# Kernel tuning notes

Hardware: AMD Instinct MI355X
Metric: run time of the kernel (lower is better)

The kernel has to match this reference:

```python
import jax, jax.numpy as jnp
import numpy as np

L, H, DK, DV, D, DH, V, S, B = 2, 12, 64, 64, 768, 3072, 32000, 1024, 2


def _layernorm(x):
    # matches custom LayerNorm: mean over last dim, biased std, no eps, no affine
    mu = jnp.mean(x, axis=-1, keepdims=True)
    sigma = jnp.sqrt(jnp.mean(jnp.square(x - mu), axis=-1, keepdims=True))
    return (x - mu) / sigma


def setup_inputs() -> dict:
    key = jax.random.key(0)
    ks = jax.random.split(key, 12)
    n = lambda k, shp: (0.02 * jax.random.normal(k, shp, dtype=jnp.float32))
    return {
        "x": jax.random.randint(ks[0], (B, S), 0, V),
        "ignore": jax.random.randint(ks[1], (B, S), 0, 2).astype(jnp.int32),
        "emb": n(ks[2], (V, D)),
        "pos": n(ks[3], (S, D)),
        "Wq": n(ks[4], (L, H, D, DK)), "bq": jnp.zeros((L, H, DK), jnp.float32),
        "Wk": n(ks[5], (L, H, D, DK)), "bk": jnp.zeros((L, H, DK), jnp.float32),
        "Wv": n(ks[6], (L, H, D, DV)), "bv": jnp.zeros((L, H, DV), jnp.float32),
        "Wo": n(ks[7], (L, H * DV, D)), "bo": jnp.zeros((L, D), jnp.float32),
        "W1": n(ks[8], (L, D, DH)), "b1": jnp.zeros((L, DH), jnp.float32),
        "W2": n(ks[9], (L, DH, D)), "b2": jnp.zeros((L, D), jnp.float32),
        "Wout": n(ks[10], (D, V)), "bout": jnp.zeros((V,), jnp.float32),
    }


def reference(x, ignore, emb, pos, Wq, bq, Wk, bk, Wv, bv, Wo, bo, W1, b1, W2, b2, Wout, bout):
    b, s = x.shape
    ign0 = (ignore == 0)  # True = valid token
    # token emb + position emb zeroed on ignored positions (dropout = eval/identity)
    h = emb[x] + pos[None, :, :] * ign0[:, :, None].astype(emb.dtype)

    # mask[b,i,j]: attend iff j<=i AND (ignore[j]==0 OR i==j)  (diagonal always kept)
    causal = jnp.tril(jnp.ones((s, s), dtype=bool))
    eye = jnp.eye(s, dtype=bool)
    allow = (ign0[:, None, None, :] | eye[None, None, :, :]) & causal[None, None, :, :]  # [b,1,i,j]

    scale = jnp.sqrt(jnp.asarray(DK, h.dtype))
    for l in range(L):
        q = jnp.einsum('bsd,hdk->bhsk', h, Wq[l]) + bq[l][None, :, None, :]
        k = jnp.einsum('bsd,hdk->bhsk', h, Wk[l]) + bk[l][None, :, None, :]
        v = jnp.einsum('bsd,hdv->bhsv', h, Wv[l]) + bv[l][None, :, None, :]
        scores = jnp.einsum('bhik,bhjk->bhij', q, k) / scale
        scores = jnp.where(allow, scores, -jnp.inf)
        p = jax.nn.softmax(scores, axis=-1)
        sa = jnp.einsum('bhij,bhjv->bhiv', p, v)
        sa = sa.transpose(0, 2, 1, 3).reshape(b, s, H * DV)  # concat heads (head-major order matches torch cat)
        attn_out = sa @ Wo[l] + bo[l]
        z = _layernorm(h + attn_out)
        # NOTE: original FeedForwardLayer applies GELU AFTER linear2 (faithful to source)
        f = jax.nn.gelu((z @ W1[l] + b1[l]) @ W2[l] + b2[l], approximate=False)
        h = _layernorm(z + f)
    return h @ Wout + bout
```

## Files before the change

kernel.cpp:

```cpp
#include <hip/hip_runtime.h>
#include <math.h>

static constexpr int L_ = 2, H_ = 12, D_ = 768, DH_ = 3072, V_ = 32000,
                     S_ = 1024, B_ = 2;
static constexpr int M_ = B_ * S_;

typedef __attribute__((ext_vector_type(4))) float f32x4;
typedef __attribute__((ext_vector_type(8))) short s16x8;
typedef __attribute__((ext_vector_type(2))) unsigned int u32x2;
typedef __attribute__((ext_vector_type(4))) unsigned int u32x4;

__device__ __forceinline__ unsigned short f2bf(float f) {
    unsigned u = __builtin_bit_cast(unsigned, f);
    u = (u + 0x7FFFu + ((u >> 16) & 1u)) >> 16;
    return (unsigned short)u;
}
__device__ __forceinline__ unsigned pack2(float a, float b) {
    return (unsigned)f2bf(a) | ((unsigned)f2bf(b) << 16);
}

__device__ __forceinline__ void gld16(const void* g, void* l) {
    __builtin_amdgcn_global_load_lds(
        (const __attribute__((address_space(1))) unsigned int*)g,
        (__attribute__((address_space(3))) unsigned int*)l, 16, 0, 0);
}

__global__ __launch_bounds__(256) void wtr_kernel(
    const float* __restrict__ in, unsigned short* __restrict__ out, int K, int N)
{
    __shared__ unsigned short t[64 * 68];
    const size_t mo = (size_t)blockIdx.z * K * N;
    in  += mo; out += mo;
    const int n0 = blockIdx.x * 64, k0 = blockIdx.y * 64;
    const int tid = threadIdx.x;
    const int kr = tid >> 2, nc = (tid & 3) * 16;
    const float* src = in + (size_t)(k0 + kr) * N + n0 + nc;
    #pragma unroll
    for (int j = 0; j < 4; ++j) {
        const float4 v = *(const float4*)(src + j * 4);
        *(u32x2*)&t[kr * 68 + nc + j * 4] = (u32x2){pack2(v.x, v.y), pack2(v.z, v.w)};
    }
    __syncthreads();
    const int nr = tid >> 2, kc = (tid & 3) * 16;
    unsigned short v16[16];
    #pragma unroll
    for (int j = 0; j < 16; ++j) v16[j] = t[(kc + j) * 68 + nr];
    unsigned short* dst = out + (size_t)(n0 + nr) * K + k0 + kc;
    ((u32x4*)dst)[0] = *(u32x4*)&v16[0];
    ((u32x4*)dst)[1] = *(u32x4*)&v16[8];
}

__global__ __launch_bounds__(256) void wtr3_kernel(
    const float* __restrict__ Wq, const float* __restrict__ Wk,
    const float* __restrict__ Wv, unsigned short* __restrict__ oq,
    unsigned short* __restrict__ ok, unsigned short* __restrict__ ov)
{
    __shared__ unsigned short t[64 * 68];
    const int z = blockIdx.z;
    const int which = z / 24, zz = z - which * 24;
    const float* in = (which == 0) ? Wq : (which == 1) ? Wk : Wv;
    unsigned short* out = (which == 0) ? oq : (which == 1) ? ok : ov;
    const size_t mo = (size_t)zz * D_ * 64;
    in += mo; out += mo;
    const int k0 = blockIdx.y * 64;
    const int tid = threadIdx.x;
    const int kr = tid >> 2, nc = (tid & 3) * 16;
    const float* src = in + (size_t)(k0 + kr) * 64 + nc;
    #pragma unroll
    for (int j = 0; j < 4; ++j) {
        const float4 v = *(const float4*)(src + j * 4);
        *(u32x2*)&t[kr * 68 + nc + j * 4] = (u32x2){pack2(v.x, v.y), pack2(v.z, v.w)};
    }
    __syncthreads();
    const int nr = tid >> 2, kc = (tid & 3) * 16;
    unsigned short v16[16];
    #pragma unroll
    for (int j = 0; j < 16; ++j) v16[j] = t[(kc + j) * 68 + nr];
    unsigned short* dst = out + (size_t)nr * D_ + k0 + kc;
    ((u32x4*)dst)[0] = *(u32x4*)&v16[0];
    ((u32x4*)dst)[1] = *(u32x4*)&v16[8];
}

__device__ __forceinline__ void xcd_decode(int& bx, int& by) {
    const int gx = gridDim.x, gy = gridDim.y;
    const int nwg = gx * gy;
    const int flat = blockIdx.y * gx + blockIdx.x;
    const int s = (flat & 7) * (nwg >> 3) + (flat >> 3);
    bx = s / gy;
    by = s % gy;
}

__device__ __forceinline__ void bt64_body(
    const unsigned short* __restrict__ A, const unsigned short* __restrict__ BT,
    const float* __restrict__ bias, void* __restrict__ Cp,
    int N, int K, int act, int k0off, int klen, int bx, int by)
{
    __shared__ unsigned short AB[12288];
    unsigned short* As = AB;
    unsigned short* Bs = AB + 4096;
    const int tid = threadIdx.x;
    const int l = tid & 63, w = tid >> 6;
    const int lq = l & 15, lg = l >> 4;
    const int brow = by * 64, bn = bx * 128;

    f32x4 acc[4][2];
    #pragma unroll
    for (int i = 0; i < 4; ++i)
        #pragma unroll
        for (int j = 0; j < 2; ++j) acc[i][j] = (f32x4)0.f;

    const int arow = tid >> 3;
    const int aq   = (tid & 7) ^ (arow & 7);
    const unsigned short* Abase = A  + (size_t)(brow + arow) * K + k0off + aq * 8;
    const unsigned short* Bbase = BT + (size_t)(bn   + arow) * K + k0off + aq * 8;

    for (int k0 = 0; k0 < klen; k0 += 64) {
        #pragma unroll
        for (int r = 0; r < 2; ++r)
            gld16(Abase + (size_t)r * 32 * K + k0, (char*)As + r * 4096 + tid * 16);
        #pragma unroll
        for (int r = 0; r < 4; ++r)
            gld16(Bbase + (size_t)r * 32 * K + k0, (char*)Bs + r * 4096 + tid * 16);
        __syncthreads();

        #pragma unroll
        for (int kk = 0; kk < 2; ++kk) {
            s16x8 af[4], bf[2];
            #pragma unroll
            for (int mf = 0; mf < 4; ++mf) {
                const int row = mf * 16 + lq;
                const int gg  = (kk * 4 + lg) ^ (row & 7);
                af[mf] = *(const s16x8*)((const char*)As + row * 128 + gg * 16);
            }
            #pragma unroll
            for (int nf = 0; nf < 2; ++nf) {
                const int col = w * 32 + nf * 16 + lq;
                const int gg  = (kk * 4 + lg) ^ (col & 7);
                bf[nf] = *(const s16x8*)((const char*)Bs + col * 128 + gg * 16);
            }
            #pragma unroll
            for (int mf = 0; mf < 4; ++mf)
                #pragma unroll
                for (int nf = 0; nf < 2; ++nf)
                    acc[mf][nf] = __builtin_amdgcn_mfma_f32_16x16x32_bf16(
                        af[mf], bf[nf], acc[mf][nf], 0, 0, 0);
        }
        __syncthreads();
    }

    if (act == 3) {
        #pragma unroll
        for (int nf = 0; nf < 2; ++nf) {
            const int c = w * 32 + nf * 16 + lq;
            const float bb = bias[bn + c];
            #pragma unroll
            for (int mf = 0; mf < 4; ++mf) {
                const int srel = mf * 16 + lg * 4;
                u32x2 pk;
                pk[0] = pack2(acc[mf][nf][0] + bb, acc[mf][nf][1] + bb);
                pk[1] = pack2(acc[mf][nf][2] + bb, acc[mf][nf][3] + bb);
                const int byo = (c * 128 + srel * 2) ^ ((c & 7) << 4);
                *(u32x2*)((char*)AB + byo) = pk;
            }
        }
        __syncthreads();
        const int row = tid >> 1, half = tid & 1;
        const int gcf = bn + row;
        const int head = gcf >> 6, d = gcf & 63;
        const int b = brow >> 10;
        const int sb = (brow & (S_ - 1)) + half * 32;
        unsigned short* dst = (unsigned short*)Cp +
            (((size_t)b * H_ + head) * 64 + d) * S_ + sb;
        #pragma unroll
        for (int u = 0; u < 4; ++u) {
            const int byo = (row * 128 + half * 64 + u * 16) ^ ((row & 7) << 4);
            ((u32x4*)dst)[u] = *(const u32x4*)((const char*)AB + byo);
        }
        return;
    }
    #pragma unroll
    for (int nf = 0; nf < 2; ++nf) {
        const int gcol = bn + w * 32 + nf * 16 + lq;
        const float bb = (act == 4) ? 0.f : bias[gcol];
        #pragma unroll
        for (int mf = 0; mf < 4; ++mf)
            #pragma unroll
            for (int rg = 0; rg < 4; ++rg) {
                const int grow = brow + mf * 16 + lg * 4 + rg;
                float vv = acc[mf][nf][rg] + bb;
                if (act == 1) vv = 0.5f * vv * (1.0f + erff(vv * 0.70710678118654752f));
                if (act == 2)
                    ((unsigned short*)Cp)[(size_t)grow * N + gcol] = f2bf(vv);
                else
                    ((float*)Cp)[(size_t)grow * N + gcol] = vv;
            }
    }
}

__global__ __launch_bounds__(256) void gemm_bt64(
    const unsigned short* __restrict__ A, const unsigned short* __restrict__ BT,
    const float* __restrict__ bias, void* __restrict__ C, int N, int K, int act)
{
    int bx, by; xcd_decode(bx, by);
    bt64_body(A, BT, bias, C, N, K, act, 0, K, bx, by);
}

__global__ __launch_bounds__(256) void gemm_qkv64(
    const unsigned short* __restrict__ A,
    const unsigned short* __restrict__ qT, const unsigned short* __restrict__ kT,
    const unsigned short* __restrict__ vT,
    const float* __restrict__ bq, const float* __restrict__ bk, const float* __restrict__ bv,
    unsigned short* __restrict__ q, unsigned short* __restrict__ k,
    unsigned short* __restrict__ v)
{
    const unsigned short* BT; const float* bi; unsigned short* C; int act;
    if (blockIdx.z == 0)      { BT = qT; bi = bq; C = q; act = 2; }
    else if (blockIdx.z == 1) { BT = kT; bi = bk; C = k; act = 2; }
    else                      { BT = vT; bi = bv; C = v; act = 3; }
    int bx, by; xcd_decode(bx, by);
    bt64_body(A, BT, bi, C, 768, 768, act, 0, 768, bx, by);
}

__global__ __launch_bounds__(256) void gemm_w2sk(
    const unsigned short* __restrict__ A, const unsigned short* __restrict__ BT,
    const float* __restrict__ bias, float* __restrict__ C0, float* __restrict__ C1)
{
    int bx, by; xcd_decode(bx, by);
    if (blockIdx.z == 0)
        bt64_body(A, BT, bias, C0, 768, DH_, 0, 0, 1536, bx, by);
    else
        bt64_body(A, BT, bias, C1, 768, DH_, 4, 1536, 1536, bx, by);
}

__global__ __launch_bounds__(256) void gemm_wosk(
    const unsigned short* __restrict__ A, const unsigned short* __restrict__ BT,
    const float* __restrict__ bias, float* __restrict__ C0, float* __restrict__ C1)
{
    int bx, by; xcd_decode(bx, by);
    if (blockIdx.z == 0)
        bt64_body(A, BT, bias, C0, 768, 768, 0, 0, 384, bx, by);
    else
        bt64_body(A, BT, bias, C1, 768, 768, 4, 384, 384, bx, by);
}

__global__ __launch_bounds__(512, 2) void gemm_deep(
    const unsigned short* __restrict__ A, const unsigned short* __restrict__ BT,
    const float* __restrict__ bias, float* __restrict__ C, int N, int K)
{
    __shared__ char lds[131072];
    const int tid = threadIdx.x;
    const int l = tid & 63, w = tid >> 6;
    const int wr = w >> 2, wc = w & 3;
    const int lq = l & 15, lg = l >> 4;

    int bx, by;
    {
        const int gx = gridDim.x, gy = gridDim.y;
        const int nwg = gx * gy;
        const int flat = blockIdx.y * gx + blockIdx.x;
        const int s = (flat & 7) * (nwg >> 3) + (flat >> 3);
        bx = s / gy; by = s % gy;
    }
    const int brow = by * 256, bn = bx * 256;
    const int NT = K >> 6;

    const int srow = (w << 3) + (l >> 3);
    const int sgr  = (l & 7) ^ (l >> 3);
    const size_t soff = (size_t)srow * K + sgr * 8;
    const unsigned short* Ag = A  + (size_t)brow * K + soff;
    const unsigned short* Bg = BT + (size_t)bn   * K + soff;
    const size_t r64  = (size_t)64 * K;
    const size_t r128 = (size_t)128 * K;
    char* const dA = lds + w * 1024;
    char* const dB = lds + 65536 + w * 1024;

#define STG_A(CB, HF, KT) do {                                                   \
    gld16(Ag + (size_t)(HF) * r128 + (size_t)(KT) * 64,                          \
          dA + (CB) * 32768 + (HF) * 16384);                                     \
    gld16(Ag + (size_t)(HF) * r128 + r64 + (size_t)(KT) * 64,                    \
          dA + (CB) * 32768 + (HF) * 16384 + 8192); } while (0)
#define STG_B(CB, HF, KT) do {                                                   \
    gld16(Bg + (size_t)(HF) * r128 + (size_t)(KT) * 64,                          \
          dB + (CB) * 32768 + (HF) * 16384);                                     \
    gld16(Bg + (size_t)(HF) * r128 + r64 + (size_t)(KT) * 64,                    \
          dB + (CB) * 32768 + (HF) * 16384 + 8192); } while (0)

    f32x4 acc[8][4];
    #pragma unroll
    for (int i = 0; i < 8; ++i)
        #pragma unroll
        for (int j = 0; j < 4; ++j) acc[i][j] = (f32x4)0.f;

    STG_A(0, 0, 0); STG_A(0, 1, 0); STG_B(0, 0, 0); STG_B(0, 1, 0);
    STG_A(1, 0, 1); STG_B(1, 0, 1);
    asm volatile("s_waitcnt vmcnt(4)" ::: "memory");
    __builtin_amdgcn_s_barrier();

    for (int t = 0; t < NT; ++t) {
        const int c = t & 1;
        const char* Ab = lds + c * 32768;
        const char* Bb = lds + 65536 + c * 32768;
        s16x8 af[4], bf[4];

        #pragma unroll
        for (int mf = 0; mf < 4; ++mf) {
            const int row = wr * 128 + mf * 16 + lq;
            af[mf] = *(const s16x8*)(Ab + row * 128 + ((lg ^ (row & 7)) << 4));
        }
        #pragma unroll
        for (int nf = 0; nf < 4; ++nf) {
            const int col = wc * 64 + nf * 16 + lq;
            bf[nf] = *(const s16x8*)(Bb + col * 128 + ((lg ^ (col & 7)) << 4));
        }
        if (t + 1 < NT) STG_A(c ^ 1, 1, t + 1);
        asm volatile("s_waitcnt lgkmcnt(0)" ::: "memory");
        __builtin_amdgcn_sched_barrier(0);
        __builtin_amdgcn_s_barrier();
        __builtin_amdgcn_s_setprio(1);
        #pragma unroll
        for (int mf = 0; mf < 4; ++mf)
            #pragma unroll
            for (int nf = 0; nf < 4; ++nf)
                acc[mf][nf] = __builtin_amdgcn_mfma_f32_16x16x32_bf16(
                    af[mf], bf[nf], acc[mf][nf], 0, 0, 0);
        __builtin_amdgcn_s_setprio(0);
        __builtin_amdgcn_s_barrier();

        #pragma unroll
        for (int mf = 0; mf < 4; ++mf) {
            const int row = wr * 128 + (mf + 4) * 16 + lq;
            af[mf] = *(const s16x8*)(Ab + row * 128 + ((lg ^ (row & 7)) << 4));
        }
        if (t + 1 < NT) STG_B(c ^ 1, 1, t + 1);
        asm volatile("s_waitcnt lgkmcnt(0)" ::: "memory");
        __builtin_amdgcn_sched_barrier(0);
        __builtin_amdgcn_s_barrier();
        __builtin_amdgcn_s_setprio(1);
        #pragma unroll
        for (int mf = 0; mf < 4; ++mf)
            #pragma unroll
            for (int nf = 0; nf < 4; ++nf)
                acc[mf + 4][nf] = __builtin_amdgcn_mfma_f32_16x16x32_bf16(
                    af[mf], bf[nf], acc[mf + 4][nf], 0, 0, 0);
        __builtin_amdgcn_s_setprio(0);
        __builtin_amdgcn_s_barrier();

        #pragma unroll
        for (int mf = 0; mf < 4; ++mf) {
            const int row = wr * 128 + mf * 16 + lq;
            af[mf] = *(const s16x8*)(Ab + row * 128 + (((4 + lg) ^ (row & 7)) << 4));
        }
        #pragma unroll
        for (int nf = 0; nf < 4; ++nf) {
            const int col = wc * 64 + nf * 16 + lq;
            bf[nf] = *(const s16x8*)(Bb + col * 128 + (((4 + lg) ^ (col & 7)) << 4));
        }
        asm volatile("s_waitcnt lgkmcnt(0)" ::: "memory");
        __builtin_amdgcn_sched_barrier(0);
        __builtin_amdgcn_s_barrier();
        __builtin_amdgcn_s_setprio(1);
        #pragma unroll
        for (int mf = 0; mf < 4; ++mf)
            #pragma unroll
            for (int nf = 0; nf < 4; ++nf)
                acc[mf][nf] = __builtin_amdgcn_mfma_f32_16x16x32_bf16(
                    af[mf], bf[nf], acc[mf][nf], 0, 0, 0);
        __builtin_amdgcn_s_setprio(0);
        __builtin_amdgcn_s_barrier();

        #pragma unroll
        for (int mf = 0; mf < 4; ++mf) {
            const int row = wr * 128 + (mf + 4) * 16 + lq;
            af[mf] = *(const s16x8*)(Ab + row * 128 + (((4 + lg) ^ (row & 7)) << 4));
        }
        asm volatile("s_waitcnt lgkmcnt(0)" ::: "memory");
        __builtin_amdgcn_sched_barrier(0);
        __builtin_amdgcn_s_barrier();
        __builtin_amdgcn_s_setprio(1);
        #pragma unroll
        for (int mf = 0; mf < 4; ++mf)
            #pragma unroll
            for (int nf = 0; nf < 4; ++nf)
                acc[mf + 4][nf] = __builtin_amdgcn_mfma_f32_16x16x32_bf16(
                    af[mf], bf[nf], acc[mf + 4][nf], 0, 0, 0);
        __builtin_amdgcn_s_setprio(0);

        if (t + 2 < NT) {
            STG_A(c, 0, t + 2); STG_B(c, 0, t + 2);
            asm volatile("s_waitcnt vmcnt(4)" ::: "memory");
            __builtin_amdgcn_s_barrier();
        } else if (t + 1 < NT) {
            asm volatile("s_waitcnt vmcnt(0)" ::: "memory");
            __builtin_amdgcn_s_barrier();
        }
    }
#undef STG_A
#undef STG_B

    #pragma unroll
    for (int nf = 0; nf < 4; ++nf) {
        const int gcol = bn + wc * 64 + nf * 16 + lq;
        const float bb = bias[gcol];
        #pragma unroll
        for (int mf = 0; mf < 8; ++mf)
            #pragma unroll
            for (int rg = 0; rg < 4; ++rg) {
                const int grow = brow + wr * 128 + mf * 16 + lg * 4 + rg;
                C[(size_t)grow * N + gcol] = acc[mf][nf][rg] + bb;
            }
    }
}

__global__ __launch_bounds__(256) void gemm_f32b(
    const unsigned short* __restrict__ A, const float* __restrict__ B,
    const float* __restrict__ bias, float* __restrict__ C, int N, int K)
{
    __shared__ unsigned short As[8192];
    __shared__ unsigned short Bs[8192];
    const int tid = threadIdx.x;
    const int l   = tid & 63, wid = tid >> 6;
    const int wr  = wid >> 1, wc = wid & 1;
    const int brow = blockIdx.y * 128, bn = blockIdx.x * 128;
    f32x4 acc[4][4];
    #pragma unroll
    for (int i = 0; i < 4; ++i)
        #pragma unroll
        for (int j = 0; j < 4; ++j) acc[i][j] = (f32x4)0.f;
    const int arow = tid >> 3;
    const int aq   = (tid & 7) ^ (arow & 7);
    const int bkq  = tid >> 5, bnq = tid & 31;
    for (int k0 = 0; k0 < K; k0 += 64) {
        #pragma unroll
        for (int r = 0; r < 4; ++r)
            gld16(A + (size_t)(brow + r * 32 + arow) * K + k0 + aq * 8,
                  (char*)As + r * 4096 + wid * 1024);
        #pragma unroll
        for (int r = 0; r < 2; ++r) {
            const int kb = r * 32 + bkq * 4;
            const float* pp = B + (size_t)(k0 + kb) * N + bn + bnq * 4;
            const float4 v0 = *(const float4*)(pp);
            const float4 v1 = *(const float4*)(pp + N);
            const float4 v2 = *(const float4*)(pp + 2 * (size_t)N);
            const float4 v3 = *(const float4*)(pp + 3 * (size_t)N);
            const int g = kb >> 3, bytek = (kb & 4) * 2;
            const float* f0 = (const float*)&v0; const float* f1 = (const float*)&v1;
            const float* f2 = (const float*)&v2; const float* f3 = (const float*)&v3;
            #pragma unroll
            for (int i = 0; i < 4; ++i) {
                const int n = bnq * 4 + i;
                char* dst = (char*)Bs + n * 128 + ((g ^ (n & 7)) * 16) + bytek;
                *(u32x2*)dst = (u32x2){pack2(f0[i], f1[i]), pack2(f2[i], f3[i])};
            }
        }
        __syncthreads();
        #pragma unroll
        for (int kk = 0; kk < 2; ++kk) {
            s16x8 af[4], bf[4];
            #pragma unroll
            for (int mf = 0; mf < 4; ++mf) {
                const int row = wr * 64 + mf * 16 + (l & 15);
                const int gg  = (kk * 4 + (l >> 4)) ^ (row & 7);
                af[mf] = *(const s16x8*)((const char*)As + row * 128 + gg * 16);
            }
            #pragma unroll
            for (int nf = 0; nf < 4; ++nf) {
                const int col = wc * 64 + nf * 16 + (l & 15);
                const int gg  = (kk * 4 + (l >> 4)) ^ (col & 7);
                bf[nf] = *(const s16x8*)((const char*)Bs + col * 128 + gg * 16);
            }
            #pragma unroll
            for (int mf = 0; mf < 4; ++mf)
                #pragma unroll
                for (int nf = 0; nf < 4; ++nf)
                    acc[mf][nf] = __builtin_amdgcn_mfma_f32_16x16x32_bf16(
                        af[mf], bf[nf], acc[mf][nf], 0, 0, 0);
        }
        __syncthreads();
    }
    const int lr = l >> 4, lc = l & 15;
    #pragma unroll
    for (int nf = 0; nf < 4; ++nf) {
        const int gcol = bn + wc * 64 + nf * 16 + lc;
        const float bb = bias[gcol];
        #pragma unroll
        for (int mf = 0; mf < 4; ++mf)
            #pragma unroll
            for (int rg = 0; rg < 4; ++rg) {
                const int grow = brow + wr * 64 + mf * 16 + lr * 4 + rg;
                C[(size_t)grow * N + gcol] = acc[mf][nf][rg] + bb;
            }
    }
}

__global__ __launch_bounds__(256) void fattn_kernel(
    const unsigned short* __restrict__ qm, const unsigned short* __restrict__ km,
    const unsigned short* __restrict__ vt, const int* __restrict__ ign,
    unsigned short* __restrict__ sab)
{
    __shared__ unsigned short Ks[2][4096];
    __shared__ unsigned short VTs[2][4096];
    __shared__ float addvs[2][64];
    __shared__ unsigned short PTs[4][1024];

    const int hh = blockIdx.y, b = blockIdx.z;
    const int zy = b * 12 + hh;
    const int qt = (zy >= 16) ? (15 - blockIdx.x) : blockIdx.x;

    const int tid = threadIdx.x;
    const int l = tid & 63, w = tid >> 6;
    const int g = l >> 4, lq = l & 15;
    const int i = qt * 64 + w * 16 + lq;

    const size_t qgb = ((size_t)(b * S_ + i)) * D_ + hh * 64;
    const s16x8 qf0 = *(const s16x8*)(qm + qgb + g * 8);
    const s16x8 qf1 = *(const s16x8*)(qm + qgb + 32 + g * 8);

    f32x4 accO[4];
    #pragma unroll
    for (int d = 0; d < 4; ++d) accO[d] = (f32x4)0.f;
    float mrun = -1e30f, lrun = 0.f;

    const int srow = tid >> 3, sg = tid & 7;
    const size_t kbase = (size_t)(b * S_) * D_ + hh * 64;
    const size_t vbase = ((size_t)(b * H_ + hh) * 64) * S_;

    auto stage = [&](int t, int bufi) {
        const int j0 = t * 64;
        #pragma unroll
        for (int r = 0; r < 2; ++r) {
            const int row = r * 32 + srow;
            const int gsw = (sg ^ (row & 7)) * 8;
            gld16(km + kbase + (size_t)(j0 + row) * D_ + gsw,
                  (char*)&Ks[bufi][0] + (r * 256 + tid) * 16);
            gld16(vt + vbase + (size_t)row * S_ + j0 + gsw,
                  (char*)&VTs[bufi][0] + (r * 256 + tid) * 16);
        }
        if (tid < 64)
            addvs[bufi][tid] = (ign[b * S_ + j0 + tid] == 0) ? 0.f : -INFINITY;
    };

    stage(0, 0);
    asm volatile("s_waitcnt vmcnt(0) lgkmcnt(0)" ::: "memory");
    __syncthreads();

    for (int t = 0; t <= qt; ++t) {
        const int cur = t & 1;
        const int j0 = t * 64;
        if (t < qt) stage(t + 1, cur ^ 1);

        f32x4 adv[4];
        #pragma unroll
        for (int kf = 0; kf < 4; ++kf)
            adv[kf] = *(const f32x4*)&addvs[cur][kf * 16 + g * 4];

        f32x4 sacc[4];
        #pragma unroll
        for (int kf = 0; kf < 4; ++kf) sacc[kf] = (f32x4)0.f;
        __builtin_amdgcn_s_setprio(1);
        #pragma unroll
        for (int kk = 0; kk < 2; ++kk) {
            const s16x8 qv = kk ? qf1 : qf0;
            #pragma unroll
            for (int kf = 0; kf < 4; ++kf) {
                const int row = kf * 16 + lq;
                const s16x8 kv = *(const s16x8*)((const char*)&Ks[cur][0] + row * 128 +
                                                 (((kk * 4 + g) ^ (row & 7)) * 16));
                sacc[kf] = __builtin_amdgcn_mfma_f32_16x16x32_bf16(kv, qv, sacc[kf], 0, 0, 0);
            }
        }
        __builtin_amdgcn_s_setprio(0);

        float tmax = -INFINITY;
        if (t < qt) {
            #pragma unroll
            for (int kf = 0; kf < 4; ++kf)
                #pragma unroll
                for (int rg = 0; rg < 4; ++rg) {
                    const float s = fmaf(sacc[kf][rg], 0.125f, adv[kf][rg]);
                    sacc[kf][rg] = s;
                    tmax = fmaxf(tmax, s);
                }
        } else {
            #pragma unroll
            for (int kf = 0; kf < 4; ++kf)
                #pragma unroll
                for (int rg = 0; rg < 4; ++rg) {
                    const int j = j0 + kf * 16 + g * 4 + rg;
                    const float sv = sacc[kf][rg] * 0.125f;
                    const float s = (j > i) ? -INFINITY
                                  : (j == i ? sv : sv + adv[kf][rg]);
                    sacc[kf][rg] = s;
                    tmax = fmaxf(tmax, s);
                }
        }
        tmax = fmaxf(tmax, __shfl_xor(tmax, 16));
        tmax = fmaxf(tmax, __shfl_xor(tmax, 32));
        const float mnew = fmaxf(mrun, tmax);
        const float fac = __expf(mrun - mnew);
        float psum = 0.f;
        #pragma unroll
        for (int kf = 0; kf < 4; ++kf)
            #pragma unroll
            for (int rg = 0; rg < 4; ++rg) {
                const float p = __expf(sacc[kf][rg] - mnew);
                sacc[kf][rg] = p;
                psum += p;
            }
        psum += __shfl_xor(psum, 16);
        psum += __shfl_xor(psum, 32);
        lrun = lrun * fac + psum;
        mrun = mnew;
        #pragma unroll
        for (int d = 0; d < 4; ++d) accO[d] *= fac;

        char* ptw = (char*)&PTs[w][0];
        #pragma unroll
        for (int kf = 0; kf < 4; ++kf) {
            u32x2 pk;
            pk[0] = pack2(sacc[kf][0], sacc[kf][1]);
            pk[1] = pack2(sacc[kf][2], sacc[kf][3]);
            *(u32x2*)(ptw + lq * 128 +
                      (((kf * 2 + (g >> 1)) ^ (lq & 7)) * 16) + (g & 1) * 8) = pk;
        }
        __builtin_amdgcn_s_setprio(1);
        #pragma unroll
        for (int kh = 0; kh < 2; ++kh) {
            const s16x8 pb = *(const s16x8*)(ptw + lq * 128 +
                                             (((kh * 4 + g) ^ (lq & 7)) * 16));
            #pragma unroll
            for (int df = 0; df < 4; ++df) {
                const int row = df * 16 + lq;
                const s16x8 vf = *(const s16x8*)((const char*)&VTs[cur][0] + row * 128 +
                                                 (((kh * 4 + g) ^ (row & 7)) * 16));
                accO[df] = __builtin_amdgcn_mfma_f32_16x16x32_bf16(vf, pb, accO[df], 0, 0, 0);
            }
        }
        __builtin_amdgcn_s_setprio(0);
        asm volatile("s_waitcnt vmcnt(0)" ::: "memory");
        __syncthreads();
    }

    const float inv = 1.0f / lrun;
    unsigned short* orow = sab + ((size_t)(b * S_ + i)) * D_ + hh * 64;
    #pragma unroll
    for (int df = 0; df < 4; ++df) {
        u32x2 pk;
        pk[0] = pack2(accO[df][0] * inv, accO[df][1] * inv);
        pk[1] = pack2(accO[df][2] * inv, accO[df][3] * inv);
        *(u32x2*)(orow + df * 16 + g * 4) = pk;
    }
}

__global__ __launch_bounds__(256) void embed_kernel(
    const int* __restrict__ x, const int* __restrict__ ign,
    const float* __restrict__ emb, const float* __restrict__ pos,
    float* __restrict__ h, unsigned short* __restrict__ hbf)
{
    const int row = blockIdx.x;
    const int s = row & (S_ - 1);
    const int tok = x[row];
    const float keep = (ign[row] == 0) ? 1.0f : 0.0f;
    const float* er = emb + (size_t)tok * D_;
    const float* pr = pos + (size_t)s * D_;
    float* hr = h + (size_t)row * D_;
    unsigned short* hb = hbf + (size_t)row * D_;
    for (int d = threadIdx.x; d < D_; d += 256) {
        const float t = er[d] + pr[d] * keep;
        hr[d] = t;
        hb[d] = f2bf(t);
    }
}

__global__ __launch_bounds__(256) void add_ln_kernel(
    const float* __restrict__ X, const float* __restrict__ Y0,
    const float* __restrict__ Y1, float* __restrict__ out,
    unsigned short* __restrict__ outbf, int mode)
{
    const int row = blockIdx.x * 4 + (threadIdx.x >> 6);
    const int l = threadIdx.x & 63;
    const float4* xr = (const float4*)(X + (size_t)row * D_);
    const float4* y0 = (const float4*)(Y0 + (size_t)row * D_);
    const float4* y1 = (const float4*)(Y1 + (size_t)row * D_);
    float4 t[3];
    float s0 = 0.f;
    #pragma unroll
    for (int k = 0; k < 3; ++k) {
        const float4 a = xr[k * 64 + l];
        float4 b = y0[k * 64 + l];
        if (mode != 0) {
            const float4 c = y1[k * 64 + l];
            b.x += c.x; b.y += c.y; b.z += c.z; b.w += c.w;
        }
        if (mode == 1) {
            b.x = 0.5f * b.x * (1.0f + erff(b.x * 0.70710678118654752f));
            b.y = 0.5f * b.y * (1.0f + erff(b.y * 0.70710678118654752f));
            b.z = 0.5f * b.z * (1.0f + erff(b.z * 0.70710678118654752f));
            b.w = 0.5f * b.w * (1.0f + erff(b.w * 0.70710678118654752f));
        }
        t[k].x = a.x + b.x; t[k].y = a.y + b.y;
        t[k].z = a.z + b.z; t[k].w = a.w + b.w;
        s0 += t[k].x + t[k].y + t[k].z + t[k].w;
    }
    #pragma unroll
    for (int o = 32; o; o >>= 1) s0 += __shfl_xor(s0, o);
    const float mu = s0 * (1.0f / D_);
    float s1 = 0.f;
    #pragma unroll
    for (int k = 0; k < 3; ++k) {
        t[k].x -= mu; t[k].y -= mu; t[k].z -= mu; t[k].w -= mu;
        s1 += t[k].x * t[k].x + t[k].y * t[k].y + t[k].z * t[k].z + t[k].w * t[k].w;
    }
    #pragma unroll
    for (int o = 32; o; o >>= 1) s1 += __shfl_xor(s1, o);
    const float inv = 1.0f / sqrtf(s1 * (1.0f / D_));
    float4* orow = (float4*)(out + (size_t)row * D_);
    u32x2* obf = (u32x2*)(outbf + (size_t)row * D_);
    #pragma unroll
    for (int k = 0; k < 3; ++k) {
        float4 r;
        r.x = t[k].x * inv; r.y = t[k].y * inv;
        r.z = t[k].z * inv; r.w = t[k].w * inv;
        orow[k * 64 + l] = r;
        u32x2 pk; pk[0] = pack2(r.x, r.y); pk[1] = pack2(r.z, r.w);
        obf[k * 64 + l] = pk;
    }
}

extern "C" void kernel_launch(void* const* d_in, const int* in_sizes, int n_in,
                              void* d_out, int out_size, void* d_ws, size_t ws_size,
                              hipStream_t stream)
{
    const int*   x    = (const int*)d_in[0];
    const int*   ign  = (const int*)d_in[1];
    const float* emb  = (const float*)d_in[2];
    const float* pos  = (const float*)d_in[3];
    const float* Wq   = (const float*)d_in[4];
    const float* bq   = (const float*)d_in[5];
    const float* Wk   = (const float*)d_in[6];
    const float* bk   = (const float*)d_in[7];
    const float* Wv   = (const float*)d_in[8];
    const float* bv   = (const float*)d_in[9];
    const float* Wo   = (const float*)d_in[10];
    const float* bo   = (const float*)d_in[11];
    const float* W1   = (const float*)d_in[12];
    const float* b1   = (const float*)d_in[13];
    const float* W2   = (const float*)d_in[14];
    const float* b2   = (const float*)d_in[15];
    const float* Wout = (const float*)d_in[16];
    const float* bout = (const float*)d_in[17];
    float* outp = (float*)d_out;

    const size_t RC = (size_t)M_ * D_;
    const size_t F1 = (size_t)M_ * DH_;
    const size_t WH = (size_t)H_ * 64 * D_;
    const size_t WF = (size_t)D_ * DH_;
    const size_t WOUTE = (size_t)V_ * D_;

    char* wsp = (char*)d_ws;
    size_t wsleft = ws_size;
    char* dop = (char*)d_out;
    auto alloc = [&](size_t bytes, bool must_ws) -> void* {
        bytes = (bytes + 255) & ~(size_t)255;
        if (wsleft >= bytes) { void* p = wsp; wsp += bytes; wsleft -= bytes; return p; }
        if (must_ws) return nullptr;
        void* p = dop; dop += bytes; return p;
    };

    unsigned short* hbf   = (unsigned short*)alloc(RC * 2, true);
    unsigned short* woutT = (unsigned short*)alloc(WOUTE * 2, true);
    float* h    = (float*)alloc(RC * 4, false);
    float* z    = (float*)alloc(RC * 4, false);
    float* tmp  = (float*)alloc(RC * 4, false);
    float* tmp1 = (float*)alloc(RC * 4, false);
    unsigned short* zbf   = (unsigned short*)alloc(RC * 2, false);
    unsigned short* sabbf = (unsigned short*)alloc(RC * 2, false);
    unsigned short* qbf   = (unsigned short*)alloc(RC * 2, false);
    unsigned short* kbf   = (unsigned short*)alloc(RC * 2, false);
    unsigned short* vtb   = (unsigned short*)alloc(RC * 2, false);
    unsigned short* f1bf  = (unsigned short*)alloc(F1 * 2, false);
    unsigned short* wqT = (unsigned short*)alloc(L_ * WH * 2, false);
    unsigned short* wkT = (unsigned short*)alloc(L_ * WH * 2, false);
    unsigned short* wvT = (unsigned short*)alloc(L_ * WH * 2, false);
    unsigned short* woT = (unsigned short*)alloc(L_ * WH * 2, false);
    unsigned short* w1T = (unsigned short*)alloc(L_ * WF * 2, false);
    unsigned short* w2T = (unsigned short*)alloc(L_ * WF * 2, false);

    embed_kernel<<<M_, 256, 0, stream>>>(x, ign, emb, pos, h, hbf);

    wtr3_kernel<<<dim3(1, 12, 72), 256, 0, stream>>>(Wq, Wk, Wv, wqT, wkT, wvT);
    wtr_kernel<<<dim3(12, 12, L_), 256, 0, stream>>>(Wo, woT, D_, D_);
    wtr_kernel<<<dim3(48, 12, L_), 256, 0, stream>>>(W1, w1T, D_, DH_);
    wtr_kernel<<<dim3(12, 48, L_), 256, 0, stream>>>(W2, w2T, DH_, D_);
    if (woutT)
        wtr_kernel<<<dim3(V_ / 64, 12, 1), 256, 0, stream>>>(Wout, woutT, D_, V_);

    for (int l = 0; l < L_; ++l) {
        gemm_qkv64<<<dim3(6, 32, 3), 256, 0, stream>>>(
            hbf, wqT + l * WH, wkT + l * WH, wvT + l * WH,
            bq + l * 768, bk + l * 768, bv + l * 768, qbf, kbf, vtb);

        fattn_kernel<<<dim3(S_ / 64, H_, B_), 256, 0, stream>>>(
            qbf, kbf, vtb, ign, sabbf);

        gemm_wosk<<<dim3(6, 32, 2), 256, 0, stream>>>(
            sabbf, woT + l * WH, bo + l * D_, tmp, tmp1);
        add_ln_kernel<<<M_ / 4, 256, 0, stream>>>(h, tmp, tmp1, z, zbf, 2);

        gemm_bt64<<<dim3(24, 32), 256, 0, stream>>>(
            zbf, w1T + l * WF, b1 + l * DH_, f1bf, DH_, D_, 2);
        gemm_w2sk<<<dim3(6, 32, 2), 256, 0, stream>>>(
            f1bf, w2T + l * WF, b2 + l * D_, tmp, tmp1);
        add_ln_kernel<<<M_ / 4, 256, 0, stream>>>(z, tmp, tmp1, h, hbf, 1);
    }

    if (woutT)
        gemm_deep<<<dim3(V_ / 256, M_ / 256), 512, 0, stream>>>(
            hbf, woutT, bout, outp, V_, D_);
    else
        gemm_f32b<<<dim3(V_ / 128, M_ / 128), 256, 0, stream>>>(
            hbf, Wout, bout, outp, V_, D_);
}
```

Before: 443.5 us.

## Process two KV tiles per iteration in attention instead of double-buffered prefetch

The flash-attention loop now loads two 64-key tiles into both LDS buffers at once, then runs QK, masking, a single online-softmax rescale and PV over the 128 keys. This halves the number of max/sum reductions, rescales and barriers per key. In exchange it drops the prefetch of the next tile during compute, so global load latency is exposed at the start of each iteration. The larger working set also raises register pressure.

```diff
diff --git a/kernel.cpp b/kernel.cpp
--- a/kernel.cpp
+++ b/kernel.cpp
@@ -539,38 +539,28 @@
             addvs[bufi][tid] = (ign[b * S_ + j0 + tid] == 0) ? 0.f : -INFINITY;
     };
 
-    stage(0, 0);
-    asm volatile("s_waitcnt vmcnt(0) lgkmcnt(0)" ::: "memory");
-    __syncthreads();
-
-    for (int t = 0; t <= qt; ++t) {
-        const int cur = t & 1;
-        const int j0 = t * 64;
-        if (t < qt) stage(t + 1, cur ^ 1);
-
-        f32x4 adv[4];
-        #pragma unroll
-        for (int kf = 0; kf < 4; ++kf)
-            adv[kf] = *(const f32x4*)&addvs[cur][kf * 16 + g * 4];
-
-        f32x4 sacc[4];
+    auto qk_sub = [&](int bufi, f32x4* sacc) {
         #pragma unroll
         for (int kf = 0; kf < 4; ++kf) sacc[kf] = (f32x4)0.f;
-        __builtin_amdgcn_s_setprio(1);
         #pragma unroll
         for (int kk = 0; kk < 2; ++kk) {
             const s16x8 qv = kk ? qf1 : qf0;
             #pragma unroll
             for (int kf = 0; kf < 4; ++kf) {
                 const int row = kf * 16 + lq;
-                const s16x8 kv = *(const s16x8*)((const char*)&Ks[cur][0] + row * 128 +
+                const s16x8 kv = *(const s16x8*)((const char*)&Ks[bufi][0] + row * 128 +
                                                  (((kk * 4 + g) ^ (row & 7)) * 16));
                 sacc[kf] = __builtin_amdgcn_mfma_f32_16x16x32_bf16(kv, qv, sacc[kf], 0, 0, 0);
             }
         }
-        __builtin_amdgcn_s_setprio(0);
-
-        float tmax = -INFINITY;
+    };
+
+    auto mask_sub = [&](int t, int bufi, f32x4* sacc, float& tmax) {
+        const int j0 = t * 64;
+        f32x4 adv[4];
+        #pragma unroll
+        for (int kf = 0; kf < 4; ++kf)
+            adv[kf] = *(const f32x4*)&addvs[bufi][kf * 16 + g * 4];
         if (t < qt) {
             #pragma unroll
             for (int kf = 0; kf < 4; ++kf)
@@ -593,26 +583,9 @@
                     tmax = fmaxf(tmax, s);
                 }
         }
-        tmax = fmaxf(tmax, __shfl_xor(tmax, 16));
-        tmax = fmaxf(tmax, __shfl_xor(tmax, 32));
-        const float mnew = fmaxf(mrun, tmax);
-        const float fac = __expf(mrun - mnew);
-        float psum = 0.f;
-        #pragma unroll
-        for (int kf = 0; kf < 4; ++kf)
-            #pragma unroll
-            for (int rg = 0; rg < 4; ++rg) {
-                const float p = __expf(sacc[kf][rg] - mnew);
-                sacc[kf][rg] = p;
-                psum += p;
-            }
-        psum += __shfl_xor(psum, 16);
-        psum += __shfl_xor(psum, 32);
-        lrun = lrun * fac + psum;
-        mrun = mnew;
-        #pragma unroll
-        for (int d = 0; d < 4; ++d) accO[d] *= fac;
-
+    };
+
+    auto pv_sub = [&](int bufi, const f32x4* sacc) {
         char* ptw = (char*)&PTs[w][0];
         #pragma unroll
         for (int kf = 0; kf < 4; ++kf) {
@@ -630,13 +603,63 @@
             #pragma unroll
             for (int df = 0; df < 4; ++df) {
                 const int row = df * 16 + lq;
-                const s16x8 vf = *(const s16x8*)((const char*)&VTs[cur][0] + row * 128 +
+                const s16x8 vf = *(const s16x8*)((const char*)&VTs[bufi][0] + row * 128 +
                                                  (((kh * 4 + g) ^ (row & 7)) * 16));
                 accO[df] = __builtin_amdgcn_mfma_f32_16x16x32_bf16(vf, pb, accO[df], 0, 0, 0);
             }
         }
         __builtin_amdgcn_s_setprio(0);
-        asm volatile("s_waitcnt vmcnt(0)" ::: "memory");
+    };
+
+    for (int tt = 0; tt <= qt; tt += 2) {
+        const bool have2 = (tt + 1 <= qt);
+        stage(tt, 0);
+        if (have2) stage(tt + 1, 1);
+        asm volatile("s_waitcnt vmcnt(0) lgkmcnt(0)" ::: "memory");
+        __syncthreads();
+
+        f32x4 sacc0[4], sacc1[4];
+        __builtin_amdgcn_s_setprio(1);
+        qk_sub(0, sacc0);
+        if (have2) qk_sub(1, sacc1);
+        __builtin_amdgcn_s_setprio(0);
+
+        float tmax = -INFINITY;
+        mask_sub(tt, 0, sacc0, tmax);
+        if (have2) mask_sub(tt + 1, 1, sacc1, tmax);
+
+        tmax = fmaxf(tmax, __shfl_xor(tmax, 16));
+        tmax = fmaxf(tmax, __shfl_xor(tmax, 32));
+        const float mnew = fmaxf(mrun, tmax);
+        const float fac = __expf(mrun - mnew);
+        float psum = 0.f;
+        #pragma unroll
+        for (int kf = 0; kf < 4; ++kf)
+            #pragma unroll
+            for (int rg = 0; rg < 4; ++rg) {
+                const float p = __expf(sacc0[kf][rg] - mnew);
+                sacc0[kf][rg] = p;
+                psum += p;
+            }
+        if (have2) {
+            #pragma unroll
+            for (int kf = 0; kf < 4; ++kf)
+                #pragma unroll
+                for (int rg = 0; rg < 4; ++rg) {
+                    const float p = __expf(sacc1[kf][rg] - mnew);
+                    sacc1[kf][rg] = p;
+                    psum += p;
+                }
+        }
+        psum += __shfl_xor(psum, 16);
+        psum += __shfl_xor(psum, 32);
+        lrun = lrun * fac + psum;
+        mrun = mnew;
+        #pragma unroll
+        for (int d = 0; d < 4; ++d) accO[d] *= fac;
+
+        pv_sub(0, sacc0);
+        if (have2) pv_sub(1, sacc1);
         __syncthreads();
     }
 
```

Measured after the change: 440.2 us. About the same (-0.8%).
